# Kernel optimization log

Hardware: AMD Instinct MI355X
Metric: run time of the kernel (lower is better)

The kernel has to match this reference:

```python
import jax, jax.numpy as jnp
import numpy as np

D_MODEL = 64
N_HEAD = 4
HEAD_DIM = D_MODEL // N_HEAD  # 16


def setup_inputs() -> dict:
    key = jax.random.key(0)
    ks = jax.random.split(key, 8)
    B, T_dec, T_enc = 16, 1024, 1024
    s = 1.0 / np.sqrt(D_MODEL)
    return {
        "x": jax.random.normal(ks[0], (B, T_dec, D_MODEL), dtype=jnp.float32),
        "encoder_outputs": jax.random.normal(ks[1], (B, T_enc, D_MODEL), dtype=jnp.float32),
        "encoder_outputs_mask": jnp.ones((B, T_enc), dtype=jnp.int32),
        "Wkv": jax.random.normal(ks[2], (D_MODEL, 2 * D_MODEL), dtype=jnp.float32) * s,
        "bkv": jnp.zeros((2 * D_MODEL,), dtype=jnp.float32),
        "Wq": jax.random.normal(ks[3], (D_MODEL, D_MODEL), dtype=jnp.float32) * s,
        "bq": jnp.zeros((D_MODEL,), dtype=jnp.float32),
        "Wproj": jax.random.normal(ks[4], (D_MODEL, D_MODEL), dtype=jnp.float32) * s,
        "bproj": jnp.zeros((D_MODEL,), dtype=jnp.float32),
    }


def reference(x, encoder_outputs, encoder_outputs_mask, Wkv, bkv, Wq, bq, Wproj, bproj):
    B, T_dec, C = x.shape
    T_enc = encoder_outputs.shape[1]
    kv = encoder_outputs @ Wkv + bkv                      # [B, T_enc, 2C]
    k, v = kv[..., :D_MODEL], kv[..., D_MODEL:]          # [B, T_enc, C]
    q = x @ Wq + bq                                      # [B, T_dec, C]
    q = q.reshape(B, T_dec, N_HEAD, HEAD_DIM)
    k = k.reshape(B, T_enc, N_HEAD, HEAD_DIM)
    v = v.reshape(B, T_enc, N_HEAD, HEAD_DIM)
    scale = 1.0 / jnp.sqrt(jnp.asarray(HEAD_DIM, dtype=q.dtype))
    att = jnp.einsum("bqhd,bkhd->bhqk", q, k) * scale    # [B, H, T_dec, T_enc]
    mask = (encoder_outputs_mask == 0)[:, None, None, :]  # [B, 1, 1, T_enc]
    att = jnp.where(mask, jnp.asarray(-jnp.inf, dtype=att.dtype), att)
    att = jax.nn.softmax(att, axis=-1)
    ctx = jnp.einsum("bhqk,bkhd->bqhd", att, v).reshape(B, T_dec, C)
    # dropout is identity at eval time
    return ctx @ Wproj + bproj
```

## Files before the change

### kernel.cpp

```cpp
#include <hip/hip_runtime.h>
#include <hip/hip_bf16.h>
#include <math.h>

#define DM 64
#define NH 4
#define HD 16
#define BATCH 16
#define TSEQ 1024

typedef short bf16x8 __attribute__((ext_vector_type(8)));
typedef short bf16x4 __attribute__((ext_vector_type(4)));
typedef float f32x4  __attribute__((ext_vector_type(4)));
typedef float f32x16 __attribute__((ext_vector_type(16)));
typedef unsigned int u32x4 __attribute__((ext_vector_type(4)));

static __device__ inline short f2bf(float x) {
    __hip_bfloat16 h = __float2bfloat16(x);
    return __builtin_bit_cast(short, h);
}
static __device__ inline float bf2f(short s) {
    __hip_bfloat16 h = __builtin_bit_cast(__hip_bfloat16, s);
    return __bfloat162float(h);
}
static __device__ inline unsigned pkbf(float a, float b) {
    unsigned r;
    asm("v_cvt_pk_bf16_f32 %0, %1, %2" : "=v"(r) : "v"(a), "v"(b));
    return r;
}

static __device__ inline void softmax_frags(const f32x16& S, bf16x8& pA0, bf16x8& pA1) {
    float p[16];
    #pragma unroll
    for (int i = 0; i < 16; ++i) p[i] = __builtin_amdgcn_exp2f(S[i]);
    unsigned a0 = pkbf(p[0],  p[1]),  b0 = pkbf(p[4],  p[5]);
    unsigned a1 = pkbf(p[2],  p[3]),  b1 = pkbf(p[6],  p[7]);
    unsigned a2 = pkbf(p[8],  p[9]),  b2 = pkbf(p[12], p[13]);
    unsigned a3 = pkbf(p[10], p[11]), b3 = pkbf(p[14], p[15]);
    asm("v_permlane32_swap_b32 %0, %1" : "+v"(a0), "+v"(b0));
    asm("v_permlane32_swap_b32 %0, %1" : "+v"(a1), "+v"(b1));
    asm("v_permlane32_swap_b32 %0, %1" : "+v"(a2), "+v"(b2));
    asm("v_permlane32_swap_b32 %0, %1" : "+v"(a3), "+v"(b3));
    u32x4 P0v; P0v[0] = a0; P0v[1] = a1; P0v[2] = b0; P0v[3] = b1;
    u32x4 P1v; P1v[0] = a2; P1v[1] = a3; P1v[2] = b2; P1v[3] = b3;
    pA0 = __builtin_bit_cast(bf16x8, P0v);
    pA1 = __builtin_bit_cast(bf16x8, P1v);
}

__global__ __launch_bounds__(256) void proj_kernel(
    const float* __restrict__ x, const float* __restrict__ enc,
    const float* __restrict__ Wkv, const float* __restrict__ bkv,
    const float* __restrict__ Wq,  const float* __restrict__ bq,
    const int* __restrict__ mask,
    short* __restrict__ qhi, short* __restrict__ qlo,
    short* __restrict__ khi, short* __restrict__ klo,
    short* __restrict__ vtt)
{
    const int t = threadIdx.x;
    const int part = blockIdx.y;
    const int r = blockIdx.x * 256 + t;
    const int b = r >> 10, trow = r & 1023;

    const float* in; const float* W; const float* bias; int cb, ldw;
    if (part < 4)      { in = x;   W = Wq;  ldw = 64;  cb = part*16;          bias = bq;  }
    else if (part < 8) { in = enc; W = Wkv; ldw = 128; cb = (part-4)*16;      bias = bkv; }
    else               { in = enc; W = Wkv; ldw = 128; cb = 64 + (part-8)*16; bias = bkv; }

    __shared__ float wsl[64][16];
    for (int idx = t; idx < 1024; idx += 256)
        wsl[idx >> 4][idx & 15] = W[(idx >> 4)*ldw + cb + (idx & 15)];

    float4 xr[16];
    const float4* inrow = (const float4*)(in + (size_t)r * 64);
    #pragma unroll
    for (int i = 0; i < 16; ++i) xr[i] = inrow[i];
    __syncthreads();

    float acc[16];
    #pragma unroll
    for (int j = 0; j < 16; ++j) acc[j] = bias[cb + j];
    #pragma unroll
    for (int k = 0; k < 64; ++k) {
        const float xv = ((const float*)xr)[k];
        const float4 w0 = ((const float4*)&wsl[k][0])[0];
        const float4 w1 = ((const float4*)&wsl[k][0])[1];
        const float4 w2 = ((const float4*)&wsl[k][0])[2];
        const float4 w3 = ((const float4*)&wsl[k][0])[3];
        acc[0]  += xv*w0.x; acc[1]  += xv*w0.y; acc[2]  += xv*w0.z; acc[3]  += xv*w0.w;
        acc[4]  += xv*w1.x; acc[5]  += xv*w1.y; acc[6]  += xv*w1.z; acc[7]  += xv*w1.w;
        acc[8]  += xv*w2.x; acc[9]  += xv*w2.y; acc[10] += xv*w2.z; acc[11] += xv*w2.w;
        acc[12] += xv*w3.x; acc[13] += xv*w3.y; acc[14] += xv*w3.z; acc[15] += xv*w3.w;
    }

    if (part < 8) {
        const float scale = (part < 4) ? 0.36067376022224085f : 1.0f;
        short* dh = (part < 4) ? qhi : khi;
        short* dl = (part < 4) ? qlo : klo;
        const int h = (part < 4) ? part : (part - 4);
        bf16x8 h0, h1, l0, l1;
        #pragma unroll
        for (int j = 0; j < 16; ++j) {
            float vf = acc[j] * scale;
            short hb = f2bf(vf);
            short lb = f2bf(vf - bf2f(hb));
            if (j < 8) { h0[j] = hb; l0[j] = lb; }
            else       { h1[j-8] = hb; l1[j-8] = lb; }
        }
        size_t off = (((size_t)(b*NH + h))*TSEQ + trow)*HD;
        *(bf16x8*)(dh + off)     = h0;
        *(bf16x8*)(dh + off + 8) = h1;
        *(bf16x8*)(dl + off)     = l0;
        *(bf16x8*)(dl + off + 8) = l1;
    } else {
        const int h = part - 8;
        const float mb = (mask[b*TSEQ + trow] != 0) ? 1.0f : 0.0f;
        short* tile = vtt + ((size_t)(b*NH + h))*32768 + (size_t)(trow >> 5)*1024;
        const int kw = trow & 31;
        #pragma unroll
        for (int j = 0; j < 16; ++j)
            tile[j*32 + kw] = f2bf(acc[j] * mb);
        tile[16*32 + kw] = (mb != 0.0f) ? (short)0x3F80 : (short)0;
    }
}

__global__ __launch_bounds__(512) void attn_kernel(
    const short* __restrict__ qhi, const short* __restrict__ qlo,
    const short* __restrict__ khi, const short* __restrict__ klo,
    const short* __restrict__ vtt,
    const float* __restrict__ Wproj, const float* __restrict__ bproj,
    float* __restrict__ out)
{
    const int tid  = threadIdx.x;
    const int lane = tid & 63;
    const int wid  = __builtin_amdgcn_readfirstlane(tid >> 6);
    const int h  = wid & 3;
    const int ks = wid >> 2;
    const int l31 = lane & 31, half = lane >> 5;

    const int bi  = blockIdx.x;
    const int xcd = bi & 7, u = bi >> 3;
    const int b     = xcd + ((u >> 4) << 3);
    const int qbase = (u & 15) * 64;

    __shared__ float Cbuf[2][64][68];
    __shared__ float Lbuf[2][NH][64];
    __shared__ u32x4 Wl[2][4][2][64];

    #pragma unroll
    for (int it = 0; it < 2; ++it) {
        const int s = tid + it*512;
        const int lane6 = s & 63;
        const int hl  = (s >> 6) & 1;
        const int stp = (s >> 7) & 3;
        const int ctc = s >> 9;
        const int c  = ctc*32 + (lane6 & 31);
        const int kb = stp*16 + (lane6 >> 5)*8;
        u32x4 wv;
        #pragma unroll
        for (int jj = 0; jj < 4; ++jj) {
            const float w0 = Wproj[(kb + 2*jj)*DM + c];
            const float w1 = Wproj[(kb + 2*jj + 1)*DM + c];
            if (hl == 0) {
                wv[jj] = pkbf(w0, w1);
            } else {
                const float h0 = bf2f(f2bf(w0));
                const float h1 = bf2f(f2bf(w1));
                wv[jj] = pkbf(w0 - h0, w1 - h1);
            }
        }
        Wl[ctc][stp][hl][lane6] = wv;
    }
    __syncthreads();

    const size_t qoff = (((size_t)(b*NH + h))*TSEQ + qbase + l31)*HD + half*8;
    const bf16x8 qAh0 = *(const bf16x8*)(qhi + qoff);
    const bf16x8 qAl0 = *(const bf16x8*)(qlo + qoff);
    const bf16x8 qAh1 = *(const bf16x8*)(qhi + qoff + 32*HD);
    const bf16x8 qAl1 = *(const bf16x8*)(qlo + qoff + 32*HD);

    const short* khb = khi + (((size_t)(b*NH + h))*TSEQ + ks*512)*HD;
    const short* klb = klo + (((size_t)(b*NH + h))*TSEQ + ks*512)*HD;
    const short* vtb = vtt + ((size_t)(b*NH + h))*32768 + (size_t)ks*16384;

    f32x16 Cacc0, Cacc1;
    #pragma unroll
    for (int i = 0; i < 16; ++i) { Cacc0[i] = 0.f; Cacc1[i] = 0.f; }

    for (int step = 0; step < 16; ++step) {
        const int ko = step * 32;
        const bf16x8 kBh = *(const bf16x8*)(khb + (size_t)(ko + l31)*HD + half*8);
        const bf16x8 kBl = *(const bf16x8*)(klb + (size_t)(ko + l31)*HD + half*8);
        const short* tile = vtb + (size_t)step * 1024;
        const bf16x8 vB0 = *(const bf16x8*)(tile + l31*32 + half*8);
        const bf16x8 vB1 = *(const bf16x8*)(tile + l31*32 + 16 + half*8);

        {
            f32x16 S;
            #pragma unroll
            for (int i = 0; i < 16; ++i) S[i] = 0.f;
            S = __builtin_amdgcn_mfma_f32_32x32x16_bf16(kBh, qAh0, S, 0, 0, 0);
            S = __builtin_amdgcn_mfma_f32_32x32x16_bf16(kBl, qAh0, S, 0, 0, 0);
            S = __builtin_amdgcn_mfma_f32_32x32x16_bf16(kBh, qAl0, S, 0, 0, 0);
            bf16x8 pA0, pA1;
            softmax_frags(S, pA0, pA1);
            Cacc0 = __builtin_amdgcn_mfma_f32_32x32x16_bf16(pA0, vB0, Cacc0, 0, 0, 0);
            Cacc0 = __builtin_amdgcn_mfma_f32_32x32x16_bf16(pA1, vB1, Cacc0, 0, 0, 0);
        }
        {
            f32x16 S;
            #pragma unroll
            for (int i = 0; i < 16; ++i) S[i] = 0.f;
            S = __builtin_amdgcn_mfma_f32_32x32x16_bf16(kBh, qAh1, S, 0, 0, 0);
            S = __builtin_amdgcn_mfma_f32_32x32x16_bf16(kBl, qAh1, S, 0, 0, 0);
            S = __builtin_amdgcn_mfma_f32_32x32x16_bf16(kBh, qAl1, S, 0, 0, 0);
            bf16x8 pA0, pA1;
            softmax_frags(S, pA0, pA1);
            Cacc1 = __builtin_amdgcn_mfma_f32_32x32x16_bf16(pA0, vB0, Cacc1, 0, 0, 0);
            Cacc1 = __builtin_amdgcn_mfma_f32_32x32x16_bf16(pA1, vB1, Cacc1, 0, 0, 0);
        }
    }

    #pragma unroll
    for (int r = 0; r < 16; ++r) {
        const int row = (r & 3) + 8*(r >> 2) + 4*half;
        if (l31 < 16) {
            Cbuf[ks][row][h*HD + l31]      = Cacc0[r];
            Cbuf[ks][32 + row][h*HD + l31] = Cacc1[r];
        } else if (l31 == 16) {
            Lbuf[ks][h][row]      = Cacc0[r];
            Lbuf[ks][h][32 + row] = Cacc1[r];
        }
    }
    __syncthreads();

    if (wid < 4) {
        const int ct = wid & 1, rt = wid >> 1;
        const int t  = rt*32 + l31;
        const int c  = ct*32 + l31;
        f32x16 D;
        const float bp = bproj[c];
        #pragma unroll
        for (int i = 0; i < 16; ++i) D[i] = bp;

        #pragma unroll
        for (int stp = 0; stp < 4; ++stp) {
            const float linv = 1.0f / (Lbuf[0][stp][t] + Lbuf[1][stp][t]);
            const int ib = stp*16 + half*8;
            const float4 x0 = *(const float4*)&Cbuf[0][t][ib];
            const float4 x1 = *(const float4*)&Cbuf[0][t][ib+4];
            const float4 y0 = *(const float4*)&Cbuf[1][t][ib];
            const float4 y1 = *(const float4*)&Cbuf[1][t][ib+4];
            float cv[8];
            cv[0] = (x0.x+y0.x)*linv; cv[1] = (x0.y+y0.y)*linv;
            cv[2] = (x0.z+y0.z)*linv; cv[3] = (x0.w+y0.w)*linv;
            cv[4] = (x1.x+y1.x)*linv; cv[5] = (x1.y+y1.y)*linv;
            cv[6] = (x1.z+y1.z)*linv; cv[7] = (x1.w+y1.w)*linv;
            u32x4 Ahv, Alv;
            #pragma unroll
            for (int jj = 0; jj < 4; ++jj) {
                const unsigned hw = pkbf(cv[2*jj], cv[2*jj+1]);
                const float h0 = bf2f((short)(hw & 0xffff));
                const float h1 = bf2f((short)(hw >> 16));
                Ahv[jj] = hw;
                Alv[jj] = pkbf(cv[2*jj] - h0, cv[2*jj+1] - h1);
            }
            const bf16x8 Ah = __builtin_bit_cast(bf16x8, Ahv);
            const bf16x8 Al = __builtin_bit_cast(bf16x8, Alv);
            const bf16x8 Bh = __builtin_bit_cast(bf16x8, Wl[ct][stp][0][lane]);
            const bf16x8 Bl = __builtin_bit_cast(bf16x8, Wl[ct][stp][1][lane]);
            D = __builtin_amdgcn_mfma_f32_32x32x16_bf16(Ah, Bh, D, 0, 0, 0);
            D = __builtin_amdgcn_mfma_f32_32x32x16_bf16(Ah, Bl, D, 0, 0, 0);
            D = __builtin_amdgcn_mfma_f32_32x32x16_bf16(Al, Bh, D, 0, 0, 0);
        }
        float* orow = out + ((size_t)b*TSEQ + qbase + rt*32)*DM + c;
        #pragma unroll
        for (int r = 0; r < 16; ++r) {
            const int tr = (r & 3) + 8*(r >> 2) + 4*half;
            orow[(size_t)tr * DM] = D[r];
        }
    }
}

extern "C" void kernel_launch(void* const* d_in, const int* in_sizes, int n_in,
                              void* d_out, int out_size, void* d_ws, size_t ws_size,
                              hipStream_t stream) {
    const float* x     = (const float*)d_in[0];
    const float* enc   = (const float*)d_in[1];
    const int*   mask  = (const int*)  d_in[2];
    const float* Wkv   = (const float*)d_in[3];
    const float* bkv   = (const float*)d_in[4];
    const float* Wq    = (const float*)d_in[5];
    const float* bq    = (const float*)d_in[6];
    const float* Wproj = (const float*)d_in[7];
    const float* bproj = (const float*)d_in[8];
    float* out = (float*)d_out;

    const size_t SZ = (size_t)BATCH*NH*TSEQ*HD;
    short* qhi = (short*)d_ws;
    short* qlo = qhi + SZ;
    short* khi = qlo + SZ;
    short* klo = khi + SZ;
    short* vtt = klo + SZ;

    proj_kernel<<<dim3(64, 12), dim3(256), 0, stream>>>(
        x, enc, Wkv, bkv, Wq, bq, mask, qhi, qlo, khi, klo, vtt);
    attn_kernel<<<dim3(256), dim3(512), 0, stream>>>(
        qhi, qlo, khi, klo, vtt, Wproj, bproj, out);
}
```

Before: 105.4 us.

## Rewrite Q/K/V projection kernel using split-bf16 MFMA instead of scalar FMA

After: 109.6 us. +4.0%, slower.

```diff
diff --git a/kernel.cpp b/kernel.cpp
--- a/kernel.cpp
+++ b/kernel.cpp
@@ -55,70 +55,121 @@
     short* __restrict__ khi, short* __restrict__ klo,
     short* __restrict__ vtt)
 {
-    const int t = threadIdx.x;
-    const int part = blockIdx.y;
-    const int r = blockIdx.x * 256 + t;
-    const int b = r >> 10, trow = r & 1023;
-
-    const float* in; const float* W; const float* bias; int cb, ldw;
-    if (part < 4)      { in = x;   W = Wq;  ldw = 64;  cb = part*16;          bias = bq;  }
-    else if (part < 8) { in = enc; W = Wkv; ldw = 128; cb = (part-4)*16;      bias = bkv; }
-    else               { in = enc; W = Wkv; ldw = 128; cb = 64 + (part-8)*16; bias = bkv; }
-
-    __shared__ float wsl[64][16];
-    for (int idx = t; idx < 1024; idx += 256)
-        wsl[idx >> 4][idx & 15] = W[(idx >> 4)*ldw + cb + (idx & 15)];
-
-    float4 xr[16];
-    const float4* inrow = (const float4*)(in + (size_t)r * 64);
-    #pragma unroll
-    for (int i = 0; i < 16; ++i) xr[i] = inrow[i];
+    const int tid  = threadIdx.x;
+    const int lane = tid & 63;
+    const int wid  = tid >> 6;
+    const int l31 = lane & 31, half = lane >> 5;
+
+    const int bi = blockIdx.x;
+    const bool isq = (bi < 128);
+    const int rowbase = (isq ? bi : bi - 128) * 128;
+    const float* in  = isq ? x : enc;
+    const int nt  = isq ? 2 : 4;
+    const int ldw = isq ? 64 : 128;
+    const float* W = isq ? Wq : Wkv;
+    const float qscale = 0.36067376022224085f;
+
+    __shared__ u32x4 Bw[4][4][2][64];
+    __shared__ float smask[128];
+
+    for (int s = tid; s < nt*512; s += 256) {
+        const int lane6 = s & 63;
+        const int hl   = (s >> 6) & 1;
+        const int ch   = (s >> 7) & 3;
+        const int tile = s >> 9;
+        const int col  = tile*32 + (lane6 & 31);
+        const int kr   = ch*16 + (lane6 >> 5)*8;
+        u32x4 wv;
+        #pragma unroll
+        for (int jj = 0; jj < 4; ++jj) {
+            float w0 = W[(kr + 2*jj)*ldw + col];
+            float w1 = W[(kr + 2*jj + 1)*ldw + col];
+            if (isq) { w0 *= qscale; w1 *= qscale; }
+            const unsigned hw = pkbf(w0, w1);
+            if (hl == 0) wv[jj] = hw;
+            else         wv[jj] = pkbf(w0 - bf2f((short)(hw & 0xffff)),
+                                       w1 - bf2f((short)(hw >> 16)));
+        }
+        Bw[tile][ch][hl][lane6] = wv;
+    }
+    if (!isq && tid < 128) {
+        const int bb = rowbase >> 10, tb = rowbase & 1023;
+        smask[tid] = (mask[bb*TSEQ + tb + tid] != 0) ? 1.0f : 0.0f;
+    }
+
+    const int rw = rowbase + wid*32;
+    const int b = rw >> 10, trow = rw & 1023;
+    const float* arow = in + (size_t)(rw + l31)*64 + half*8;
+    bf16x8 Ah[4], Al[4];
+    #pragma unroll
+    for (int c = 0; c < 4; ++c) {
+        const float4 f0 = *(const float4*)(arow + c*16);
+        const float4 f1 = *(const float4*)(arow + c*16 + 4);
+        const float v[8] = {f0.x,f0.y,f0.z,f0.w, f1.x,f1.y,f1.z,f1.w};
+        u32x4 hv, lv;
+        #pragma unroll
+        for (int jj = 0; jj < 4; ++jj) {
+            const unsigned hw = pkbf(v[2*jj], v[2*jj+1]);
+            hv[jj] = hw;
+            lv[jj] = pkbf(v[2*jj]   - bf2f((short)(hw & 0xffff)),
+                          v[2*jj+1] - bf2f((short)(hw >> 16)));
+        }
+        Ah[c] = __builtin_bit_cast(bf16x8, hv);
+        Al[c] = __builtin_bit_cast(bf16x8, lv);
+    }
     __syncthreads();
 
-    float acc[16];
-    #pragma unroll
-    for (int j = 0; j < 16; ++j) acc[j] = bias[cb + j];
-    #pragma unroll
-    for (int k = 0; k < 64; ++k) {
-        const float xv = ((const float*)xr)[k];
-        const float4 w0 = ((const float4*)&wsl[k][0])[0];
-        const float4 w1 = ((const float4*)&wsl[k][0])[1];
-        const float4 w2 = ((const float4*)&wsl[k][0])[2];
-        const float4 w3 = ((const float4*)&wsl[k][0])[3];
-        acc[0]  += xv*w0.x; acc[1]  += xv*w0.y; acc[2]  += xv*w0.z; acc[3]  += xv*w0.w;
-        acc[4]  += xv*w1.x; acc[5]  += xv*w1.y; acc[6]  += xv*w1.z; acc[7]  += xv*w1.w;
-        acc[8]  += xv*w2.x; acc[9]  += xv*w2.y; acc[10] += xv*w2.z; acc[11] += xv*w2.w;
-        acc[12] += xv*w3.x; acc[13] += xv*w3.y; acc[14] += xv*w3.z; acc[15] += xv*w3.w;
-    }
-
-    if (part < 8) {
-        const float scale = (part < 4) ? 0.36067376022224085f : 1.0f;
-        short* dh = (part < 4) ? qhi : khi;
-        short* dl = (part < 4) ? qlo : klo;
-        const int h = (part < 4) ? part : (part - 4);
-        bf16x8 h0, h1, l0, l1;
-        #pragma unroll
-        for (int j = 0; j < 16; ++j) {
-            float vf = acc[j] * scale;
-            short hb = f2bf(vf);
-            short lb = f2bf(vf - bf2f(hb));
-            if (j < 8) { h0[j] = hb; l0[j] = lb; }
-            else       { h1[j-8] = hb; l1[j-8] = lb; }
-        }
-        size_t off = (((size_t)(b*NH + h))*TSEQ + trow)*HD;
-        *(bf16x8*)(dh + off)     = h0;
-        *(bf16x8*)(dh + off + 8) = h1;
-        *(bf16x8*)(dl + off)     = l0;
-        *(bf16x8*)(dl + off + 8) = l1;
-    } else {
-        const int h = part - 8;
-        const float mb = (mask[b*TSEQ + trow] != 0) ? 1.0f : 0.0f;
-        short* tile = vtt + ((size_t)(b*NH + h))*32768 + (size_t)(trow >> 5)*1024;
-        const int kw = trow & 31;
-        #pragma unroll
-        for (int j = 0; j < 16; ++j)
-            tile[j*32 + kw] = f2bf(acc[j] * mb);
-        tile[16*32 + kw] = (mb != 0.0f) ? (short)0x3F80 : (short)0;
+    for (int tile = 0; tile < nt; ++tile) {
+        const int col = tile*32 + l31;
+        const float bv = isq ? bq[col]*qscale : bkv[col];
+        f32x16 D;
+        #pragma unroll
+        for (int i = 0; i < 16; ++i) D[i] = bv;
+        #pragma unroll
+        for (int c = 0; c < 4; ++c) {
+            const bf16x8 Bh = __builtin_bit_cast(bf16x8, Bw[tile][c][0][lane]);
+            const bf16x8 Bl = __builtin_bit_cast(bf16x8, Bw[tile][c][1][lane]);
+            D = __builtin_amdgcn_mfma_f32_32x32x16_bf16(Ah[c], Bh, D, 0, 0, 0);
+            D = __builtin_amdgcn_mfma_f32_32x32x16_bf16(Ah[c], Bl, D, 0, 0, 0);
+            D = __builtin_amdgcn_mfma_f32_32x32x16_bf16(Al[c], Bh, D, 0, 0, 0);
+        }
+
+        if (isq || tile < 2) {
+            short* dh = isq ? qhi : khi;
+            short* dl = isq ? qlo : klo;
+            const int head = col >> 4;
+            const int d    = col & 15;
+            const size_t base = (((size_t)(b*NH + head))*TSEQ + trow)*HD + d;
+            #pragma unroll
+            for (int r = 0; r < 16; ++r) {
+                const int m = (r & 3) + 8*(r >> 2) + 4*half;
+                const float vf = D[r];
+                const short hb = f2bf(vf);
+                dh[base + (size_t)m*HD] = hb;
+                dl[base + (size_t)m*HD] = f2bf(vf - bf2f(hb));
+            }
+        } else {
+            const int vcol = col - 64;
+            const int head = vcol >> 4, d = vcol & 15;
+            short* tp = vtt + ((size_t)(b*NH + head))*32768 + (size_t)(trow >> 5)*1024;
+            unsigned* tp32 = (unsigned*)tp;
+            #pragma unroll
+            for (int r = 0; r < 16; r += 2) {
+                const int m = (r & 3) + 8*(r >> 2) + 4*half;
+                const float mb0 = smask[wid*32 + m];
+                const float mb1 = smask[wid*32 + m + 1];
+                tp32[(d*32 + m) >> 1] = pkbf(D[r]*mb0, D[r+1]*mb1);
+            }
+            if (d == 0) {
+                #pragma unroll
+                for (int r = 0; r < 16; r += 2) {
+                    const int m = (r & 3) + 8*(r >> 2) + 4*half;
+                    const unsigned o0 = (smask[wid*32+m]   != 0.f) ? 0x3F80u : 0u;
+                    const unsigned o1 = (smask[wid*32+m+1] != 0.f) ? 0x3F80u : 0u;
+                    tp32[(16*32 + m) >> 1] = o0 | (o1 << 16);
+                }
+            }
+        }
     }
 }
 
@@ -301,7 +352,7 @@
     short* klo = khi + SZ;
     short* vtt = klo + SZ;
 
-    proj_kernel<<<dim3(64, 12), dim3(256), 0, stream>>>(
+    proj_kernel<<<dim3(256), dim3(256), 0, stream>>>(
         x, enc, Wkv, bkv, Wq, bq, mask, qhi, qlo, khi, klo, vtt);
     attn_kernel<<<dim3(256), dim3(512), 0, stream>>>(
         qhi, qlo, khi, klo, vtt, Wproj, bproj, out);
```
